# Performance work log

Hardware: AMD Instinct MI355X
Metric: run time of the kernel (lower is better)

Reference implementation:

```python
import jax, jax.numpy as jnp
import numpy as np

B, T, D, DO = 8, 2048, 1024, 1024

def setup_inputs() -> dict:
    key = jax.random.key(0)
    ks = jax.random.split(key, 7)
    s = 1.0 / np.sqrt(D)
    return {
        "input_tensor": jax.random.normal(ks[0], (B, T, D), dtype=jnp.float32),
        "Wq": jax.random.uniform(ks[1], (D, D), jnp.float32, -s, s),
        "bq": jax.random.uniform(ks[2], (D,), jnp.float32, -s, s),
        "Wk": jax.random.uniform(ks[3], (D, D), jnp.float32, -s, s),
        "bk": jax.random.uniform(ks[4], (D,), jnp.float32, -s, s),
        "Wv": jax.random.uniform(ks[5], (D, DO), jnp.float32, -s, s),
        "bv": jax.random.uniform(ks[6], (DO,), jnp.float32, -s, s),
    }

def reference(input_tensor, Wq, bq, Wk, bk, Wv, bv):
    scale = jnp.sqrt(jnp.float32(input_tensor.shape[-1]))
    q = input_tensor @ Wq + bq            # [B,T,D]
    k = input_tensor @ Wk + bk            # [B,T,D]
    v = input_tensor @ Wv + bv            # [B,T,DO]
    scores = jnp.einsum('btd,bsd->bts', q, k) / scale  # [B,T,T]
    attn = jax.nn.softmax(scores, axis=-1)
    return jnp.einsum('bts,bso->bto', attn, v)         # [B,T,DO]
```

## Files before the change

kernel.cpp:

```cpp
#include <hip/hip_runtime.h>
#include <stdint.h>

typedef unsigned short u16;
typedef __attribute__((ext_vector_type(4))) float    floatx4;
typedef __attribute__((ext_vector_type(8))) __bf16   bf16x8;
typedef __attribute__((ext_vector_type(2))) unsigned int uintx2;
typedef __attribute__((ext_vector_type(4))) unsigned int uintx4;

__device__ inline u16 f2bf(float f) {
  unsigned int u = __builtin_bit_cast(unsigned int, f);
  u += 0x7fffu + ((u >> 16) & 1u);
  return (u16)(u >> 16);
}

#define GLD16(gsrc, ldst)                                                        \
  __builtin_amdgcn_global_load_lds(                                              \
      (__attribute__((address_space(1))) void*)(gsrc),                           \
      (__attribute__((address_space(3))) void*)(ldst), 16, 0, 0)

#define SB() __builtin_amdgcn_sched_barrier(0)

__global__ __launch_bounds__(256) void prep_kernel(const float* __restrict__ x,
                                                   const float* __restrict__ Wq,
                                                   const float* __restrict__ Wk,
                                                   const float* __restrict__ Wv,
                                                   u16* __restrict__ xb,
                                                   u16* __restrict__ WT) {
  const int z = blockIdx.z;
  const int tid = threadIdx.y * 32 + threadIdx.x;
  if (z >= 3) {
    long blk = (long)(z - 3) * 1024 + blockIdx.y * 32 + blockIdx.x;
    long i = (blk * 256 + tid) * 8;
    floatx4 a = *(const floatx4*)(x + i);
    floatx4 b = *(const floatx4*)(x + i + 4);
    uintx4 o;
    o[0] = (unsigned)f2bf(a[0]) | ((unsigned)f2bf(a[1]) << 16);
    o[1] = (unsigned)f2bf(a[2]) | ((unsigned)f2bf(a[3]) << 16);
    o[2] = (unsigned)f2bf(b[0]) | ((unsigned)f2bf(b[1]) << 16);
    o[3] = (unsigned)f2bf(b[2]) | ((unsigned)f2bf(b[3]) << 16);
    *(uintx4*)(xb + i) = o;
    return;
  }
  __shared__ float tile[32][33];
  const float* W = (z == 0) ? Wq : (z == 1) ? Wk : Wv;
  u16* dst = WT + (long)z * 1024 * 1024;
  int bx = blockIdx.x * 32, by = blockIdx.y * 32;
  int tx = threadIdx.x, ty = threadIdx.y;
  for (int i = 0; i < 32; i += 8)
    tile[ty + i][tx] = W[(long)(by + ty + i) * 1024 + bx + tx];
  __syncthreads();
  for (int i = 0; i < 32; i += 8)
    dst[(long)(bx + ty + i) * 1024 + by + tx] = f2bf(tile[tx][ty + i]);
}

#define BM 256
#define BN 256
#define BK 64

template <int MODE, int GN>
__global__ __launch_bounds__(1024, 4)
void gemm_bt(const u16* __restrict__ Aall, const u16* __restrict__ Ball,
             void* __restrict__ Call, void* __restrict__ C2,
             const float* __restrict__ bias, const float* __restrict__ bias2,
             float* __restrict__ lsum,
             int M, int N, int K, long aStride, long bStride, long cStride) {
  __shared__ __align__(16) u16 As[2][BM * BK];
  __shared__ __align__(16) u16 Bs[2][BN * BK];

  const int z = blockIdx.z;
  const u16* A  = Aall + (long)z * aStride;
  const u16* Bt = Ball + (long)z * bStride;

  int m_idx, n_idx;
  {
    const int tiles_n = gridDim.x, tiles_m = gridDim.y;
    int nwg = tiles_n * tiles_m;
    int bid = blockIdx.y * tiles_n + blockIdx.x;
    int qq = nwg >> 3;
    int L = (bid & 7) * qq + (bid >> 3);
    int per_group = GN * tiles_m;
    int g = L / per_group;
    int rem = L - g * per_group;
    n_idx = g * GN + rem % GN;
    m_idx = rem / GN;
  }

  const int tid  = threadIdx.x;
  const int m0   = m_idx * BM;
  const int n0   = n_idx * BN;
  const int wave = tid >> 6;
  const int lane = tid & 63;
  const int wm   = (wave >> 2) * 64;
  const int wn   = (wave & 3) * 64;
  const int l15  = lane & 15;
  const int quad = lane >> 4;

  floatx4 acc[4][4];
  floatx4 zero = {0.f, 0.f, 0.f, 0.f};
#pragma unroll
  for (int i = 0; i < 4; ++i)
#pragma unroll
    for (int j = 0; j < 4; ++j) acc[i][j] = zero;

  const int swz   = (quad ^ (l15 & 7)) * 8;
  const int aOff0 = (wm + l15) * 64 + swz;
  const int bOff0 = (wn + l15) * 64 + swz;

  const u16* gA[2];
  const u16* gB[2];
#pragma unroll
  for (int i = 0; i < 2; ++i) {
    int ci = i * 1024 + tid;
    int r = ci >> 3, sc = ci & 7;
    int col = (sc ^ (r & 7)) * 8;
    gA[i] = A  + (long)(m0 + r) * K + col;
    gB[i] = Bt + (long)(n0 + r) * K + col;
  }

  const int nt = K / BK;

  {
    u16* lA = (u16*)As + tid * 8;
    u16* lB = (u16*)Bs + tid * 8;
    GLD16(gA[0], lA); GLD16(gA[1], lA + 8192);
    GLD16(gB[0], lB); GLD16(gB[1], lB + 8192);
    GLD16(gA[0] + BK, lA + 16384); GLD16(gA[1] + BK, lA + 24576);
    GLD16(gB[0] + BK, lB + 16384); GLD16(gB[1] + BK, lB + 24576);
  }
  SB();
  asm volatile("s_waitcnt vmcnt(4)" ::: "memory");
  SB();
  __builtin_amdgcn_s_barrier();
  SB();
#pragma unroll
  for (int i = 0; i < 2; ++i) { gA[i] += 2 * BK; gB[i] += 2 * BK; }

  for (int t = 0; t < nt; ++t) {
    const int bo  = (t & 1) << 14;
    const u16* aP0 = (const u16*)As + bo + aOff0;
    const u16* bP0 = (const u16*)Bs + bo + bOff0;
    const u16* aP1 = (const u16*)As + bo + (aOff0 ^ 32);
    const u16* bP1 = (const u16*)Bs + bo + (bOff0 ^ 32);
    u16* ldsA = (u16*)As + bo + tid * 8;
    u16* ldsB = (u16*)Bs + bo + tid * 8;
    bf16x8 af[4], bfr[4];

#pragma unroll
    for (int mi = 0; mi < 4; ++mi)
      af[mi] = *(const bf16x8*)(aP0 + mi * 1024);
#pragma unroll
    for (int ni = 0; ni < 4; ++ni)
      bfr[ni] = *(const bf16x8*)(bP0 + ni * 1024);
    asm volatile("s_waitcnt lgkmcnt(0)" ::: "memory");
    SB();
    __builtin_amdgcn_s_setprio(1);
#pragma unroll
    for (int mi = 0; mi < 4; ++mi)
#pragma unroll
      for (int ni = 0; ni < 4; ++ni)
        acc[mi][ni] = __builtin_amdgcn_mfma_f32_16x16x32_bf16(
            bfr[ni], af[mi], acc[mi][ni], 0, 0, 0);
    __builtin_amdgcn_s_setprio(0);
    SB();

#pragma unroll
    for (int mi = 0; mi < 4; ++mi)
      af[mi] = *(const bf16x8*)(aP1 + mi * 1024);
#pragma unroll
    for (int ni = 0; ni < 4; ++ni)
      bfr[ni] = *(const bf16x8*)(bP1 + ni * 1024);
    asm volatile("s_waitcnt lgkmcnt(0)" ::: "memory");
    SB();
    __builtin_amdgcn_s_barrier();
    SB();
    if (t + 2 < nt) {
      GLD16(gA[0], ldsA); GLD16(gA[1], ldsA + 8192);
      GLD16(gB[0], ldsB); GLD16(gB[1], ldsB + 8192);
#pragma unroll
      for (int i = 0; i < 2; ++i) { gA[i] += BK; gB[i] += BK; }
    }
    SB();
    __builtin_amdgcn_s_setprio(1);
#pragma unroll
    for (int mi = 0; mi < 4; ++mi)
#pragma unroll
      for (int ni = 0; ni < 4; ++ni)
        acc[mi][ni] = __builtin_amdgcn_mfma_f32_16x16x32_bf16(
            bfr[ni], af[mi], acc[mi][ni], 0, 0, 0);
    __builtin_amdgcn_s_setprio(0);
    SB();
    if (t + 3 <= nt - 1)      asm volatile("s_waitcnt vmcnt(4)" ::: "memory");
    else if (t + 2 == nt - 1) asm volatile("s_waitcnt vmcnt(4)" ::: "memory");
    else if (t + 1 == nt - 1) asm volatile("s_waitcnt vmcnt(0)" ::: "memory");
    SB();
    __builtin_amdgcn_s_barrier();
    SB();
  }

  if (MODE == 1) {
    u16* wbase = (wave < 8 ? (u16*)As : (u16*)Bs) + (wave & 7) * 4096;
#pragma unroll
    for (int mi = 0; mi < 4; ++mi) {
      const int dl = mi * 16 + l15;
      const float b = bias[m0 + wm + dl];
#pragma unroll
      for (int ni = 0; ni < 4; ++ni) {
        floatx4 v = acc[mi][ni];
        int tc = ni * 2 + (quad >> 1);
        int ad = dl * 64 + ((tc ^ (dl & 7)) << 3) + (quad & 1) * 4;
        uintx2 o;
        o[0] = (unsigned)f2bf(v[0] + b) | ((unsigned)f2bf(v[1] + b) << 16);
        o[1] = (unsigned)f2bf(v[2] + b) | ((unsigned)f2bf(v[3] + b) << 16);
        *(uintx2*)(wbase + ad) = o;
      }
    }
    u16* C = (u16*)Call;
    const int cb0 = n0 + wn;
    const long base0 = ((long)(cb0 >> 11) * 1024) * 2048 + (cb0 & 2047);
    const int rl = lane >> 3, cl = lane & 7;
#pragma unroll
    for (int p = 0; p < 8; ++p) {
      int r = p * 8 + rl;
      uintx4 v = *(uintx4*)(wbase + r * 64 + ((cl ^ (r & 7)) << 3));
      *(uintx4*)(C + base0 + (long)(m0 + wm + r) * 2048 + cl * 8) = v;
    }
  } else {
#pragma unroll
  for (int mi = 0; mi < 4; ++mi) {
    const int row = m0 + wm + mi * 16 + l15;
    if (MODE == 2) {
      u16* C = (u16*)Call + (long)z * cStride;
      float rs = 0.f;
#pragma unroll
      for (int ni = 0; ni < 4; ++ni) {
        int colb = n0 + wn + ni * 16 + quad * 4;
        floatx4 v = acc[mi][ni];
        float e0 = __expf(v[0] * 0.03125f), e1 = __expf(v[1] * 0.03125f);
        float e2 = __expf(v[2] * 0.03125f), e3 = __expf(v[3] * 0.03125f);
        rs += (e0 + e1) + (e2 + e3);
        uintx2 o;
        o[0] = (unsigned)f2bf(e0) | ((unsigned)f2bf(e1) << 16);
        o[1] = (unsigned)f2bf(e2) | ((unsigned)f2bf(e3) << 16);
        *(uintx2*)(C + (long)row * N + colb) = o;
      }
      rs += __shfl_xor(rs, 16);
      rs += __shfl_xor(rs, 32);
      if (quad == 0) atomicAdd(lsum + (long)z * 2048 + row, rs);
    } else if (MODE == 3) {
      float* C = (float*)Call + (long)z * cStride;
      float inv = 1.0f / lsum[(long)z * 2048 + row];
#pragma unroll
      for (int ni = 0; ni < 4; ++ni) {
        int colb = n0 + wn + ni * 16 + quad * 4;
        floatx4 v = acc[mi][ni];
        floatx4 o = {v[0] * inv, v[1] * inv, v[2] * inv, v[3] * inv};
        *(floatx4*)(C + (long)row * N + colb) = o;
      }
    } else {
#pragma unroll
      for (int ni = 0; ni < 4; ++ni) {
        int colb = n0 + wn + ni * 16 + quad * 4;
        u16* C = (colb < 1024) ? (u16*)Call : (u16*)C2;
        const float* bp = (colb < 1024) ? bias + colb : bias2 + (colb - 1024);
        floatx4 b = *(const floatx4*)bp;
        floatx4 v = acc[mi][ni];
        uintx2 o;
        o[0] = (unsigned)f2bf(v[0] + b[0]) | ((unsigned)f2bf(v[1] + b[1]) << 16);
        o[1] = (unsigned)f2bf(v[2] + b[2]) | ((unsigned)f2bf(v[3] + b[3]) << 16);
        *(uintx2*)(C + (long)row * 1024 + (colb & 1023)) = o;
      }
    }
  }
  }
}

extern "C" void kernel_launch(void* const* d_in, const int* in_sizes, int n_in,
                              void* d_out, int out_size, void* d_ws, size_t ws_size,
                              hipStream_t stream) {
  const float* x  = (const float*)d_in[0];
  const float* Wq = (const float*)d_in[1];
  const float* bq = (const float*)d_in[2];
  const float* Wk = (const float*)d_in[3];
  const float* bk = (const float*)d_in[4];
  const float* Wv = (const float*)d_in[5];
  const float* bv = (const float*)d_in[6];
  float* out = (float*)d_out;

  const long BT = 16384;
  u16* xb = (u16*)d_ws;
  u16* WT = xb + BT * 1024;
  u16* qb = WT + 3L * 1024 * 1024;
  u16* kb = qb + BT * 1024;
  u16* vT = kb + BT * 1024;
  u16* S  = vT + BT * 1024;
  float* lsum = (float*)(S + 8L * 2048 * 2048);

  hipMemsetAsync(lsum, 0, 8 * 2048 * sizeof(float), stream);

  prep_kernel<<<dim3(32, 32, 11), dim3(32, 8), 0, stream>>>(x, Wq, Wk, Wv, xb, WT);

  gemm_bt<0, 8><<<dim3(8, 64, 1), 1024, 0, stream>>>(
      xb, WT, qb, kb, bq, bk, nullptr, 16384, 2048, 1024, 0, 0, 0);
  gemm_bt<1, 8><<<dim3(64, 4, 1), 1024, 0, stream>>>(
      WT + 2L * 1024 * 1024, xb, vT, nullptr, bv, nullptr, nullptr,
      1024, 16384, 1024, 0, 0, 0);
  gemm_bt<2, 8><<<dim3(8, 8, 8), 1024, 0, stream>>>(
      qb, kb, S, nullptr, nullptr, nullptr, lsum,
      2048, 2048, 1024, 2048L * 1024, 2048L * 1024, 2048L * 2048);
  gemm_bt<3, 4><<<dim3(4, 8, 8), 1024, 0, stream>>>(
      S, vT, out, nullptr, nullptr, nullptr, lsum,
      2048, 1024, 2048, 2048L * 2048, 1024L * 2048, 2048L * 1024);
}
```

Baseline: 374.1 us.

## Shrink GEMM tiles to 128x128 with single-buffered LDS and plain syncthreads

Cuts the GEMM block tile from 256x256 with 16 waves to 128x128 with 4 waves, and changes launch bounds and grid sizes to match. The double-buffered, hand-scheduled prefetch pipeline (explicit vmcnt waits, sched barriers, setprio) is replaced by a single-buffered load-then-syncthreads loop. The smaller tiles aim for more blocks and occupancy, but they lower data reuse per tile, and global loads no longer overlap with MFMA work inside a block. The epilogue's wave-based LDS staging is cut down to fit the smaller tile; any epilogue code beyond that line is not visible here.

```diff
diff --git a/kernel.cpp b/kernel.cpp
--- a/kernel.cpp
+++ b/kernel.cpp
@@ -17,8 +17,6 @@
   __builtin_amdgcn_global_load_lds(                                              \
       (__attribute__((address_space(1))) void*)(gsrc),                           \
       (__attribute__((address_space(3))) void*)(ldst), 16, 0, 0)
-
-#define SB() __builtin_amdgcn_sched_barrier(0)
 
 __global__ __launch_bounds__(256) void prep_kernel(const float* __restrict__ x,
                                                    const float* __restrict__ Wq,
@@ -53,19 +51,19 @@
     dst[(long)(bx + ty + i) * 1024 + by + tx] = f2bf(tile[tx][ty + i]);
 }
 
-#define BM 256
-#define BN 256
+#define BM 128
+#define BN 128
 #define BK 64
 
 template <int MODE, int GN>
-__global__ __launch_bounds__(1024, 4)
+__global__ __launch_bounds__(256, 3)
 void gemm_bt(const u16* __restrict__ Aall, const u16* __restrict__ Ball,
              void* __restrict__ Call, void* __restrict__ C2,
              const float* __restrict__ bias, const float* __restrict__ bias2,
              float* __restrict__ lsum,
              int M, int N, int K, long aStride, long bStride, long cStride) {
-  __shared__ __align__(16) u16 As[2][BM * BK];
-  __shared__ __align__(16) u16 Bs[2][BN * BK];
+  __shared__ __align__(16) u16 As[BM * BK];
+  __shared__ __align__(16) u16 Bs[BN * BK];
 
   const int z = blockIdx.z;
   const u16* A  = Aall + (long)z * aStride;
@@ -90,8 +88,8 @@
   const int n0   = n_idx * BN;
   const int wave = tid >> 6;
   const int lane = tid & 63;
-  const int wm   = (wave >> 2) * 64;
-  const int wn   = (wave & 3) * 64;
+  const int wm   = (wave >> 1) * 64;
+  const int wn   = (wave & 1) * 64;
   const int l15  = lane & 15;
   const int quad = lane >> 4;
 
@@ -106,99 +104,60 @@
   const int aOff0 = (wm + l15) * 64 + swz;
   const int bOff0 = (wn + l15) * 64 + swz;
 
-  const u16* gA[2];
-  const u16* gB[2];
-#pragma unroll
-  for (int i = 0; i < 2; ++i) {
-    int ci = i * 1024 + tid;
+  const u16* gA[4];
+  const u16* gB[4];
+#pragma unroll
+  for (int i = 0; i < 4; ++i) {
+    int ci = i * 256 + tid;
     int r = ci >> 3, sc = ci & 7;
     int col = (sc ^ (r & 7)) * 8;
     gA[i] = A  + (long)(m0 + r) * K + col;
     gB[i] = Bt + (long)(n0 + r) * K + col;
   }
+  u16* lA = As + tid * 8;
+  u16* lB = Bs + tid * 8;
 
   const int nt = K / BK;
 
-  {
-    u16* lA = (u16*)As + tid * 8;
-    u16* lB = (u16*)Bs + tid * 8;
-    GLD16(gA[0], lA); GLD16(gA[1], lA + 8192);
-    GLD16(gB[0], lB); GLD16(gB[1], lB + 8192);
-    GLD16(gA[0] + BK, lA + 16384); GLD16(gA[1] + BK, lA + 24576);
-    GLD16(gB[0] + BK, lB + 16384); GLD16(gB[1] + BK, lB + 24576);
-  }
-  SB();
-  asm volatile("s_waitcnt vmcnt(4)" ::: "memory");
-  SB();
-  __builtin_amdgcn_s_barrier();
-  SB();
-#pragma unroll
-  for (int i = 0; i < 2; ++i) { gA[i] += 2 * BK; gB[i] += 2 * BK; }
-
   for (int t = 0; t < nt; ++t) {
-    const int bo  = (t & 1) << 14;
-    const u16* aP0 = (const u16*)As + bo + aOff0;
-    const u16* bP0 = (const u16*)Bs + bo + bOff0;
-    const u16* aP1 = (const u16*)As + bo + (aOff0 ^ 32);
-    const u16* bP1 = (const u16*)Bs + bo + (bOff0 ^ 32);
-    u16* ldsA = (u16*)As + bo + tid * 8;
-    u16* ldsB = (u16*)Bs + bo + tid * 8;
-    bf16x8 af[4], bfr[4];
-
-#pragma unroll
-    for (int mi = 0; mi < 4; ++mi)
-      af[mi] = *(const bf16x8*)(aP0 + mi * 1024);
+#pragma unroll
+    for (int i = 0; i < 4; ++i) {
+      GLD16(gA[i], lA + i * 2048);
+      GLD16(gB[i], lB + i * 2048);
+      gA[i] += BK; gB[i] += BK;
+    }
+    __syncthreads();
+
+    bf16x8 af0[4], bfr0[4], af1[4], bfr1[4];
+#pragma unroll
+    for (int mi = 0; mi < 4; ++mi)
+      af0[mi] = *(const bf16x8*)(As + aOff0 + mi * 1024);
 #pragma unroll
     for (int ni = 0; ni < 4; ++ni)
-      bfr[ni] = *(const bf16x8*)(bP0 + ni * 1024);
-    asm volatile("s_waitcnt lgkmcnt(0)" ::: "memory");
-    SB();
-    __builtin_amdgcn_s_setprio(1);
+      bfr0[ni] = *(const bf16x8*)(Bs + bOff0 + ni * 1024);
 #pragma unroll
     for (int mi = 0; mi < 4; ++mi)
 #pragma unroll
       for (int ni = 0; ni < 4; ++ni)
         acc[mi][ni] = __builtin_amdgcn_mfma_f32_16x16x32_bf16(
-            bfr[ni], af[mi], acc[mi][ni], 0, 0, 0);
-    __builtin_amdgcn_s_setprio(0);
-    SB();
-
-#pragma unroll
-    for (int mi = 0; mi < 4; ++mi)
-      af[mi] = *(const bf16x8*)(aP1 + mi * 1024);
+            bfr0[ni], af0[mi], acc[mi][ni], 0, 0, 0);
+#pragma unroll
+    for (int mi = 0; mi < 4; ++mi)
+      af1[mi] = *(const bf16x8*)(As + (aOff0 ^ 32) + mi * 1024);
 #pragma unroll
     for (int ni = 0; ni < 4; ++ni)
-      bfr[ni] = *(const bf16x8*)(bP1 + ni * 1024);
-    asm volatile("s_waitcnt lgkmcnt(0)" ::: "memory");
-    SB();
-    __builtin_amdgcn_s_barrier();
-    SB();
-    if (t + 2 < nt) {
-      GLD16(gA[0], ldsA); GLD16(gA[1], ldsA + 8192);
-      GLD16(gB[0], ldsB); GLD16(gB[1], ldsB + 8192);
-#pragma unroll
-      for (int i = 0; i < 2; ++i) { gA[i] += BK; gB[i] += BK; }
-    }
-    SB();
-    __builtin_amdgcn_s_setprio(1);
+      bfr1[ni] = *(const bf16x8*)(Bs + (bOff0 ^ 32) + ni * 1024);
 #pragma unroll
     for (int mi = 0; mi < 4; ++mi)
 #pragma unroll
       for (int ni = 0; ni < 4; ++ni)
         acc[mi][ni] = __builtin_amdgcn_mfma_f32_16x16x32_bf16(
-            bfr[ni], af[mi], acc[mi][ni], 0, 0, 0);
-    __builtin_amdgcn_s_setprio(0);
-    SB();
-    if (t + 3 <= nt - 1)      asm volatile("s_waitcnt vmcnt(4)" ::: "memory");
-    else if (t + 2 == nt - 1) asm volatile("s_waitcnt vmcnt(4)" ::: "memory");
-    else if (t + 1 == nt - 1) asm volatile("s_waitcnt vmcnt(0)" ::: "memory");
-    SB();
-    __builtin_amdgcn_s_barrier();
-    SB();
+            bfr1[ni], af1[mi], acc[mi][ni], 0, 0, 0);
+    __syncthreads();
   }
 
   if (MODE == 1) {
-    u16* wbase = (wave < 8 ? (u16*)As : (u16*)Bs) + (wave & 7) * 4096;
+    u16* wbase = (wave < 2 ? As : Bs) + (wave & 1) * 4096;
 #pragma unroll
     for (int mi = 0; mi < 4; ++mi) {
       const int dl = mi * 16 + l15;
@@ -299,15 +258,15 @@
 
   prep_kernel<<<dim3(32, 32, 11), dim3(32, 8), 0, stream>>>(x, Wq, Wk, Wv, xb, WT);
 
-  gemm_bt<0, 8><<<dim3(8, 64, 1), 1024, 0, stream>>>(
+  gemm_bt<0, 8><<<dim3(16, 128, 1), 256, 0, stream>>>(
       xb, WT, qb, kb, bq, bk, nullptr, 16384, 2048, 1024, 0, 0, 0);
-  gemm_bt<1, 8><<<dim3(64, 4, 1), 1024, 0, stream>>>(
+  gemm_bt<1, 8><<<dim3(128, 8, 1), 256, 0, stream>>>(
       WT + 2L * 1024 * 1024, xb, vT, nullptr, bv, nullptr, nullptr,
       1024, 16384, 1024, 0, 0, 0);
-  gemm_bt<2, 8><<<dim3(8, 8, 8), 1024, 0, stream>>>(
+  gemm_bt<2, 8><<<dim3(16, 16, 8), 256, 0, stream>>>(
       qb, kb, S, nullptr, nullptr, nullptr, lsum,
       2048, 2048, 1024, 2048L * 1024, 2048L * 1024, 2048L * 2048);
-  gemm_bt<3, 4><<<dim3(4, 8, 8), 1024, 0, stream>>>(
+  gemm_bt<3, 4><<<dim3(8, 16, 8), 256, 0, stream>>>(
       S, vT, out, nullptr, nullptr, nullptr, lsum,
       2048, 1024, 2048, 2048L * 2048, 1024L * 2048, 2048L * 1024);
 }
```

Result: slower. 381.7 us (+2.1%).
